# Kernel optimization log

Measured on AMD Instinct MI355X. Metric: run time of the kernel, lower is better.

The kernel has to match this reference:

```python
import jax, jax.numpy as jnp
import numpy as np

D_MODEL = 1024
SEQ_LEN = 32768


def setup_inputs() -> dict:
    key = jax.random.key(0)
    k1, k2, k3 = jax.random.split(key, 3)
    inputs = jax.random.normal(k1, (SEQ_LEN,), dtype=jnp.float32)
    W = jax.random.normal(k2, (D_MODEL, D_MODEL), dtype=jnp.float32) * (1.0 / np.sqrt(D_MODEL))
    b = jax.random.normal(k3, (D_MODEL,), dtype=jnp.float32) * 0.01
    return {"inputs": inputs, "W": W, "b": b}


def reference(inputs, W, b):
    d_model = W.shape[0]
    # t: [D], p: [L] -- log(1 + position)
    t = jnp.linspace(0.0, 1.0, d_model, dtype=inputs.dtype)
    p = jnp.log1p(jnp.arange(inputs.shape[0], dtype=inputs.dtype))
    # phase[l, d] = 2*pi * inputs[l] * (t[d] + p[l]); sum sin over positions
    phase = 2.0 * jnp.pi * inputs[:, None] * (t[None, :] + p[:, None])  # [L, D]
    signal = jnp.sum(jnp.sin(phase), axis=0)  # [D]
    # nn.Linear: x @ W.T + b
    return signal @ W.T + b
```

## Files before the change

### kernel.cpp

```cpp
#include <hip/hip_runtime.h>

#define L_TOTAL 32768
#define D_MODEL 1024
#define LCHUNK  64
#define NQ      (D_MODEL / 256)
#define NBLK_S  ((L_TOTAL / LCHUNK) * NQ)

__global__ __launch_bounds__(256) void signal_kernel(const float* __restrict__ x,
                                                     float* __restrict__ signal) {
    __shared__ float2 sxp[LCHUNK];
    const int tid   = threadIdx.x;
    const int q     = blockIdx.x & (NQ - 1);
    const int c     = blockIdx.x >> 2;
    const int lbase = c * LCHUNK;

    if (tid < LCHUNK) {
        const int l   = lbase + tid;
        const float xv = x[l];
        sxp[tid] = make_float2(xv, xv * __logf(1.0f + (float)l));
    }
    __syncthreads();

    const int   d = q * 256 + tid;
    const float t = (float)d * (1.0f / 1023.0f);

    float a0 = 0.f, a1 = 0.f, a2 = 0.f, a3 = 0.f;
    #pragma unroll
    for (int j = 0; j < LCHUNK; j += 4) {
        const float2 v0 = sxp[j + 0];
        const float2 v1 = sxp[j + 1];
        const float2 v2 = sxp[j + 2];
        const float2 v3 = sxp[j + 3];
        a0 += __builtin_amdgcn_sinf(__builtin_amdgcn_fractf(fmaf(v0.x, t, v0.y)));
        a1 += __builtin_amdgcn_sinf(__builtin_amdgcn_fractf(fmaf(v1.x, t, v1.y)));
        a2 += __builtin_amdgcn_sinf(__builtin_amdgcn_fractf(fmaf(v2.x, t, v2.y)));
        a3 += __builtin_amdgcn_sinf(__builtin_amdgcn_fractf(fmaf(v3.x, t, v3.y)));
    }
    atomicAdd(&signal[d], (a0 + a1) + (a2 + a3));
}

__global__ __launch_bounds__(256) void matvec_kernel(const float* __restrict__ W,
                                                     const float* __restrict__ b,
                                                     const float* __restrict__ signal,
                                                     float* __restrict__ out) {
    const int wave = threadIdx.x >> 6;
    const int lane = threadIdx.x & 63;
    const int row  = blockIdx.x * 4 + wave;

    const float4* Wr = (const float4*)(W + (size_t)row * D_MODEL);
    const float4* S  = (const float4*)signal;

    float sum = 0.f;
    #pragma unroll
    for (int k = 0; k < 4; ++k) {
        const float4 w4 = Wr[lane + 64 * k];
        const float4 s4 = S[lane + 64 * k];
        sum += w4.x * s4.x + w4.y * s4.y + w4.z * s4.z + w4.w * s4.w;
    }
    #pragma unroll
    for (int off = 32; off > 0; off >>= 1)
        sum += __shfl_down(sum, off, 64);
    if (lane == 0) out[row] = sum + b[row];
}

extern "C" void kernel_launch(void* const* d_in, const int* in_sizes, int n_in,
                              void* d_out, int out_size, void* d_ws, size_t ws_size,
                              hipStream_t stream) {
    const float* x = (const float*)d_in[0];
    const float* W = (const float*)d_in[1];
    const float* b = (const float*)d_in[2];
    float* out    = (float*)d_out;
    float* signal = (float*)d_ws;

    hipMemsetAsync(signal, 0, D_MODEL * sizeof(float), stream);
    signal_kernel<<<NBLK_S, 256, 0, stream>>>(x, signal);
    matvec_kernel<<<D_MODEL / 4, 256, 0, stream>>>(W, b, signal, out);
}
```

Measured before the change: 76.57 us.

## Replace atomic accumulation with partial-sum buffer plus deterministic reduce kernel

The signal kernel now writes per-chunk partial sums to a workspace buffer instead of issuing atomicAdds. A new reduce kernel sums those partials per output dimension. This also removes the memset. Chunk size doubles to halve the number of partials, and the matvec splits each row across two waves with 512-thread blocks. The cost is an extra kernel launch plus about 1 MB of partial-sum traffic. The larger chunk also halves the signal-kernel grid, which reduces parallelism.

```diff
diff --git a/kernel.cpp b/kernel.cpp
--- a/kernel.cpp
+++ b/kernel.cpp
@@ -2,12 +2,13 @@
 
 #define L_TOTAL 32768
 #define D_MODEL 1024
-#define LCHUNK  64
+#define LCHUNK  128
+#define NCH     (L_TOTAL / LCHUNK)
 #define NQ      (D_MODEL / 256)
-#define NBLK_S  ((L_TOTAL / LCHUNK) * NQ)
+#define NBLK_S  (NCH * NQ)
 
 __global__ __launch_bounds__(256) void signal_kernel(const float* __restrict__ x,
-                                                     float* __restrict__ signal) {
+                                                     float* __restrict__ part) {
     __shared__ float2 sxp[LCHUNK];
     const int tid   = threadIdx.x;
     const int q     = blockIdx.x & (NQ - 1);
@@ -36,23 +37,43 @@
         a2 += __builtin_amdgcn_sinf(__builtin_amdgcn_fractf(fmaf(v2.x, t, v2.y)));
         a3 += __builtin_amdgcn_sinf(__builtin_amdgcn_fractf(fmaf(v3.x, t, v3.y)));
     }
-    atomicAdd(&signal[d], (a0 + a1) + (a2 + a3));
+    part[c * D_MODEL + d] = (a0 + a1) + (a2 + a3);
 }
 
-__global__ __launch_bounds__(256) void matvec_kernel(const float* __restrict__ W,
+__global__ __launch_bounds__(256) void reduce_kernel(const float* __restrict__ part,
+                                                     float* __restrict__ signal) {
+    __shared__ float red[4][64];
+    const int tid = threadIdx.x;
+    const int dd  = blockIdx.x * 64 + (tid & 63);
+    const int s   = tid >> 6;
+    float acc = 0.f;
+    #pragma unroll 8
+    for (int j = 0; j < NCH / 4; ++j)
+        acc += part[(s * (NCH / 4) + j) * D_MODEL + dd];
+    red[s][tid & 63] = acc;
+    __syncthreads();
+    if (tid < 64)
+        signal[blockIdx.x * 64 + tid] =
+            (red[0][tid] + red[1][tid]) + (red[2][tid] + red[3][tid]);
+}
+
+__global__ __launch_bounds__(512) void matvec_kernel(const float* __restrict__ W,
                                                      const float* __restrict__ b,
                                                      const float* __restrict__ signal,
                                                      float* __restrict__ out) {
-    const int wave = threadIdx.x >> 6;
-    const int lane = threadIdx.x & 63;
-    const int row  = blockIdx.x * 4 + wave;
+    __shared__ float rsum[8];
+    const int tid  = threadIdx.x;
+    const int wv   = tid >> 6;
+    const int lane = tid & 63;
+    const int row  = blockIdx.x * 4 + (wv >> 1);
+    const int h    = wv & 1;
 
     const float4* Wr = (const float4*)(W + (size_t)row * D_MODEL);
     const float4* S  = (const float4*)signal;
 
     float sum = 0.f;
     #pragma unroll
-    for (int k = 0; k < 4; ++k) {
+    for (int k = h * 2; k < h * 2 + 2; ++k) {
         const float4 w4 = Wr[lane + 64 * k];
         const float4 s4 = S[lane + 64 * k];
         sum += w4.x * s4.x + w4.y * s4.y + w4.z * s4.z + w4.w * s4.w;
@@ -60,7 +81,12 @@
     #pragma unroll
     for (int off = 32; off > 0; off >>= 1)
         sum += __shfl_down(sum, off, 64);
-    if (lane == 0) out[row] = sum + b[row];
+    if (lane == 0) rsum[wv] = sum;
+    __syncthreads();
+    if (tid < 4) {
+        const int r = blockIdx.x * 4 + tid;
+        out[r] = rsum[2 * tid] + rsum[2 * tid + 1] + b[r];
+    }
 }
 
 extern "C" void kernel_launch(void* const* d_in, const int* in_sizes, int n_in,
@@ -70,9 +96,10 @@
     const float* W = (const float*)d_in[1];
     const float* b = (const float*)d_in[2];
     float* out    = (float*)d_out;
-    float* signal = (float*)d_ws;
+    float* part   = (float*)d_ws;
+    float* signal = part + NCH * D_MODEL;
 
-    hipMemsetAsync(signal, 0, D_MODEL * sizeof(float), stream);
-    signal_kernel<<<NBLK_S, 256, 0, stream>>>(x, signal);
-    matvec_kernel<<<D_MODEL / 4, 256, 0, stream>>>(W, b, signal, out);
+    signal_kernel<<<NBLK_S, 256, 0, stream>>>(x, part);
+    reduce_kernel<<<D_MODEL / 64, 256, 0, stream>>>(part, signal);
+    matvec_kernel<<<D_MODEL / 4, 512, 0, stream>>>(W, b, signal, out);
 }
```

Measured after the change: 70.41 us. 1.09x faster.

## Fuse signal and matvec into one persistent kernel with grid barriers

Applied to the files above, without the earlier changes.

Replaces the memset, the atomic-accumulating signal kernel and the separate matvec kernel with a single launch of 512 blocks of 512 threads. Blocks write per-chunk partial sums to workspace, and after a software grid barrier half the blocks reduce the partials deterministically into the signal vector. After a second barrier every block computes two output rows, with W rows prefetched before the first barrier. This removes launch overhead and atomics, but relies on all 512 blocks being co-resident and adds a global partial buffer round trip plus spin-wait barriers.

```diff
diff --git a/kernel.cpp b/kernel.cpp
--- a/kernel.cpp
+++ b/kernel.cpp
@@ -2,31 +2,59 @@
 
 #define L_TOTAL 32768
 #define D_MODEL 1024
-#define LCHUNK  64
-#define NQ      (D_MODEL / 256)
-#define NBLK_S  ((L_TOTAL / LCHUNK) * NQ)
+#define NBLK    512
+#define NTHR    512
+#define LCH     128
+#define NCH     (L_TOTAL / LCH)
 
-__global__ __launch_bounds__(256) void signal_kernel(const float* __restrict__ x,
-                                                     float* __restrict__ signal) {
-    __shared__ float2 sxp[LCHUNK];
-    const int tid   = threadIdx.x;
-    const int q     = blockIdx.x & (NQ - 1);
-    const int c     = blockIdx.x >> 2;
-    const int lbase = c * LCHUNK;
+__device__ unsigned int g_bar = 0u;
 
-    if (tid < LCHUNK) {
-        const int l   = lbase + tid;
+__device__ __forceinline__ void grid_sync() {
+    __syncthreads();
+    if (threadIdx.x == 0) {
+        const unsigned int ticket =
+            __hip_atomic_fetch_add(&g_bar, 1u, __ATOMIC_RELEASE, __HIP_MEMORY_SCOPE_AGENT);
+        const unsigned int target = (ticket & ~(unsigned int)(NBLK - 1)) + NBLK;
+        while ((int)(__hip_atomic_load(&g_bar, __ATOMIC_RELAXED,
+                                       __HIP_MEMORY_SCOPE_AGENT) - target) < 0)
+            __builtin_amdgcn_s_sleep(2);
+        __builtin_amdgcn_fence(__ATOMIC_ACQUIRE, "agent");
+    }
+    __syncthreads();
+}
+
+__global__ __launch_bounds__(NTHR, 4) void fused_kernel(const float* __restrict__ x,
+                                                        const float* __restrict__ W,
+                                                        const float* __restrict__ b,
+                                                        float* __restrict__ out,
+                                                        float* __restrict__ ws) {
+    __shared__ float2 sxp[LCH];
+    __shared__ float  wsum[8][4];
+    __shared__ float  rsum[8];
+
+    float* part   = ws;
+    float* signal = ws + NCH * D_MODEL;
+
+    const int tid  = threadIdx.x;
+    const int blk  = blockIdx.x;
+    const int lane = tid & 63;
+    const int wv   = tid >> 6;
+
+    const int c = blk >> 1;
+    const int h = blk & 1;
+    if (tid < LCH) {
+        const int l = c * LCH + tid;
         const float xv = x[l];
         sxp[tid] = make_float2(xv, xv * __logf(1.0f + (float)l));
     }
     __syncthreads();
 
-    const int   d = q * 256 + tid;
+    const int   d = h * 512 + tid;
     const float t = (float)d * (1.0f / 1023.0f);
 
     float a0 = 0.f, a1 = 0.f, a2 = 0.f, a3 = 0.f;
     #pragma unroll
-    for (int j = 0; j < LCHUNK; j += 4) {
+    for (int j = 0; j < LCH; j += 4) {
         const float2 v0 = sxp[j + 0];
         const float2 v1 = sxp[j + 1];
         const float2 v2 = sxp[j + 2];
@@ -36,31 +64,47 @@
         a2 += __builtin_amdgcn_sinf(__builtin_amdgcn_fractf(fmaf(v2.x, t, v2.y)));
         a3 += __builtin_amdgcn_sinf(__builtin_amdgcn_fractf(fmaf(v3.x, t, v3.y)));
     }
-    atomicAdd(&signal[d], (a0 + a1) + (a2 + a3));
-}
+    part[c * D_MODEL + d] = (a0 + a1) + (a2 + a3);
 
-__global__ __launch_bounds__(256) void matvec_kernel(const float* __restrict__ W,
-                                                     const float* __restrict__ b,
-                                                     const float* __restrict__ signal,
-                                                     float* __restrict__ out) {
-    const int wave = threadIdx.x >> 6;
-    const int lane = threadIdx.x & 63;
-    const int row  = blockIdx.x * 4 + wave;
+    const int   q    = wv & 3;
+    const int   row  = 2 * blk + (wv >> 2);
+    const float4 w4  = ((const float4*)(W + (size_t)row * D_MODEL))[q * 64 + lane];
 
-    const float4* Wr = (const float4*)(W + (size_t)row * D_MODEL);
-    const float4* S  = (const float4*)signal;
+    grid_sync();
 
-    float sum = 0.f;
-    #pragma unroll
-    for (int k = 0; k < 4; ++k) {
-        const float4 w4 = Wr[lane + 64 * k];
-        const float4 s4 = S[lane + 64 * k];
-        sum += w4.x * s4.x + w4.y * s4.y + w4.z * s4.z + w4.w * s4.w;
+    if (blk < NBLK / 2) {
+        const int d0 = blk * 4;
+        const int di = tid & 3;
+        const int c0 = tid >> 2;
+        float a = part[c0 * D_MODEL + d0 + di]
+                + part[(c0 + 128) * D_MODEL + d0 + di];
+        a += __shfl_xor(a, 4, 64);
+        a += __shfl_xor(a, 8, 64);
+        a += __shfl_xor(a, 16, 64);
+        a += __shfl_xor(a, 32, 64);
+        if (lane < 4) wsum[wv][lane] = a;
+        __syncthreads();
+        if (tid < 4)
+            signal[d0 + tid] = ((wsum[0][tid] + wsum[1][tid]) +
+                                (wsum[2][tid] + wsum[3][tid])) +
+                               ((wsum[4][tid] + wsum[5][tid]) +
+                                (wsum[6][tid] + wsum[7][tid]));
     }
+
+    grid_sync();
+
+    const float4 s4 = ((const float4*)signal)[q * 64 + lane];
+    float sum = w4.x * s4.x + w4.y * s4.y + w4.z * s4.z + w4.w * s4.w;
     #pragma unroll
     for (int off = 32; off > 0; off >>= 1)
         sum += __shfl_down(sum, off, 64);
-    if (lane == 0) out[row] = sum + b[row];
+    if (lane == 0) rsum[wv] = sum;
+    __syncthreads();
+    if (tid < 2) {
+        const int r = 2 * blk + tid;
+        out[r] = ((rsum[4 * tid] + rsum[4 * tid + 1]) +
+                  (rsum[4 * tid + 2] + rsum[4 * tid + 3])) + b[r];
+    }
 }
 
 extern "C" void kernel_launch(void* const* d_in, const int* in_sizes, int n_in,
@@ -70,9 +114,7 @@
     const float* W = (const float*)d_in[1];
     const float* b = (const float*)d_in[2];
     float* out    = (float*)d_out;
-    float* signal = (float*)d_ws;
+    float* ws     = (float*)d_ws;
 
-    hipMemsetAsync(signal, 0, D_MODEL * sizeof(float), stream);
-    signal_kernel<<<NBLK_S, 256, 0, stream>>>(x, signal);
-    matvec_kernel<<<D_MODEL / 4, 256, 0, stream>>>(W, b, signal, out);
+    fused_kernel<<<NBLK, NTHR, 0, stream>>>(x, W, b, out, ws);
 }
```

Result: slower. 126.5 us (+65.2%).

## Replace atomic signal accumulation with per-chunk partials reduced in matvec kernel

Applied to the files above, without the earlier changes.

The signal kernel now gives each block 512 positions and 128 d-values, and splits the positions across two halves of the block. It writes per-chunk partial sums to workspace instead of issuing global atomicAdds, which removes the memset launch and the atomic contention. The matvec kernel now reduces the 64 partials per d in every block before doing the dot product. This is redundant work across 256 blocks, and it drops the grid from 2048 to 512 blocks.

```diff
diff --git a/kernel.cpp b/kernel.cpp
--- a/kernel.cpp
+++ b/kernel.cpp
@@ -2,65 +2,102 @@
 
 #define L_TOTAL 32768
 #define D_MODEL 1024
-#define LCHUNK  64
-#define NQ      (D_MODEL / 256)
-#define NBLK_S  ((L_TOTAL / LCHUNK) * NQ)
+#define NCH     64
+#define LCH     (L_TOTAL / NCH)
+#define NBLK_S  (NCH * 8)
 
 __global__ __launch_bounds__(256) void signal_kernel(const float* __restrict__ x,
-                                                     float* __restrict__ signal) {
-    __shared__ float2 sxp[LCHUNK];
-    const int tid   = threadIdx.x;
-    const int q     = blockIdx.x & (NQ - 1);
-    const int c     = blockIdx.x >> 2;
-    const int lbase = c * LCHUNK;
+                                                     float* __restrict__ part) {
+    __shared__ float2 sxp[LCH];
+    __shared__ float  hred[256];
+    const int tid = threadIdx.x;
+    const int c   = blockIdx.x >> 3;
+    const int q   = blockIdx.x & 7;
 
-    if (tid < LCHUNK) {
-        const int l   = lbase + tid;
-        const float xv = x[l];
-        sxp[tid] = make_float2(xv, xv * __logf(1.0f + (float)l));
+    {
+        const int l0 = c * LCH + tid;
+        const float x0 = x[l0], x1 = x[l0 + 256];
+        sxp[tid]       = make_float2(x0, x0 * __logf(1.0f + (float)l0));
+        sxp[tid + 256] = make_float2(x1, x1 * __logf(1.0f + (float)(l0 + 256)));
     }
     __syncthreads();
 
-    const int   d = q * 256 + tid;
-    const float t = (float)d * (1.0f / 1023.0f);
+    const int   dl = tid & 127;
+    const int   h  = tid >> 7;
+    const float t  = (float)(q * 128 + dl) * (1.0f / 1023.0f);
 
     float a0 = 0.f, a1 = 0.f, a2 = 0.f, a3 = 0.f;
-    #pragma unroll
-    for (int j = 0; j < LCHUNK; j += 4) {
-        const float2 v0 = sxp[j + 0];
-        const float2 v1 = sxp[j + 1];
-        const float2 v2 = sxp[j + 2];
-        const float2 v3 = sxp[j + 3];
+    #pragma unroll 4
+    for (int j = 0; j < 256; j += 4) {
+        const float2 v0 = sxp[h * 256 + j + 0];
+        const float2 v1 = sxp[h * 256 + j + 1];
+        const float2 v2 = sxp[h * 256 + j + 2];
+        const float2 v3 = sxp[h * 256 + j + 3];
         a0 += __builtin_amdgcn_sinf(__builtin_amdgcn_fractf(fmaf(v0.x, t, v0.y)));
         a1 += __builtin_amdgcn_sinf(__builtin_amdgcn_fractf(fmaf(v1.x, t, v1.y)));
         a2 += __builtin_amdgcn_sinf(__builtin_amdgcn_fractf(fmaf(v2.x, t, v2.y)));
         a3 += __builtin_amdgcn_sinf(__builtin_amdgcn_fractf(fmaf(v3.x, t, v3.y)));
     }
-    atomicAdd(&signal[d], (a0 + a1) + (a2 + a3));
+    hred[tid] = (a0 + a1) + (a2 + a3);
+    __syncthreads();
+    if (tid < 128)
+        part[c * D_MODEL + q * 128 + tid] = hred[tid] + hred[128 + tid];
 }
 
-__global__ __launch_bounds__(256) void matvec_kernel(const float* __restrict__ W,
-                                                     const float* __restrict__ b,
-                                                     const float* __restrict__ signal,
-                                                     float* __restrict__ out) {
-    const int wave = threadIdx.x >> 6;
-    const int lane = threadIdx.x & 63;
-    const int row  = blockIdx.x * 4 + wave;
+__global__ __launch_bounds__(1024) void finish_kernel(const float* __restrict__ W,
+                                                      const float* __restrict__ b,
+                                                      const float* __restrict__ part,
+                                                      float* __restrict__ out) {
+    __shared__ float4 red[4][256];
+    __shared__ float4 ssig[256];
+    __shared__ float  rsum[16];
 
-    const float4* Wr = (const float4*)(W + (size_t)row * D_MODEL);
-    const float4* S  = (const float4*)signal;
+    const int tid = threadIdx.x;
+    const int blk = blockIdx.x;
 
-    float sum = 0.f;
-    #pragma unroll
-    for (int k = 0; k < 4; ++k) {
-        const float4 w4 = Wr[lane + 64 * k];
-        const float4 s4 = S[lane + 64 * k];
-        sum += w4.x * s4.x + w4.y * s4.y + w4.z * s4.z + w4.w * s4.w;
+    {
+        const int dq = tid & 255;
+        const int cs = tid >> 8;
+        const float4* p4 = (const float4*)part;
+        float4 A = make_float4(0.f, 0.f, 0.f, 0.f);
+        float4 B = make_float4(0.f, 0.f, 0.f, 0.f);
+        #pragma unroll
+        for (int j = 0; j < 16; j += 2) {
+            const float4 u = p4[(cs * 16 + j) * 256 + dq];
+            const float4 v = p4[(cs * 16 + j + 1) * 256 + dq];
+            A.x += u.x; A.y += u.y; A.z += u.z; A.w += u.w;
+            B.x += v.x; B.y += v.y; B.z += v.z; B.w += v.w;
+        }
+        A.x += B.x; A.y += B.y; A.z += B.z; A.w += B.w;
+        red[cs][dq] = A;
     }
+    __syncthreads();
+    if (tid < 256) {
+        const float4 r0 = red[0][tid], r1 = red[1][tid];
+        const float4 r2 = red[2][tid], r3 = red[3][tid];
+        ssig[tid] = make_float4((r0.x + r1.x) + (r2.x + r3.x),
+                                (r0.y + r1.y) + (r2.y + r3.y),
+                                (r0.z + r1.z) + (r2.z + r3.z),
+                                (r0.w + r1.w) + (r2.w + r3.w));
+    }
+    __syncthreads();
+
+    const int  wv   = tid >> 6;
+    const int  lane = tid & 63;
+    const int  q    = wv & 3;
+    const int  rl   = wv >> 2;
+    const int  row  = blk * 4 + rl;
+    const float4 w4 = ((const float4*)(W + (size_t)row * D_MODEL))[q * 64 + lane];
+    const float4 s4 = ssig[q * 64 + lane];
+    float sum = w4.x * s4.x + w4.y * s4.y + w4.z * s4.z + w4.w * s4.w;
     #pragma unroll
     for (int off = 32; off > 0; off >>= 1)
         sum += __shfl_down(sum, off, 64);
-    if (lane == 0) out[row] = sum + b[row];
+    if (lane == 0) rsum[wv] = sum;
+    __syncthreads();
+    if (tid < 4)
+        out[blk * 4 + tid] = ((rsum[tid * 4] + rsum[tid * 4 + 1]) +
+                              (rsum[tid * 4 + 2] + rsum[tid * 4 + 3])) + b[blk * 4 + tid];
 }
 
 extern "C" void kernel_launch(void* const* d_in, const int* in_sizes, int n_in,
@@ -70,9 +107,8 @@
     const float* W = (const float*)d_in[1];
     const float* b = (const float*)d_in[2];
     float* out    = (float*)d_out;
-    float* signal = (float*)d_ws;
+    float* part   = (float*)d_ws;
 
-    hipMemsetAsync(signal, 0, D_MODEL * sizeof(float), stream);
-    signal_kernel<<<NBLK_S, 256, 0, stream>>>(x, signal);
-    matvec_kernel<<<D_MODEL / 4, 256, 0, stream>>>(W, b, signal, out);
+    signal_kernel<<<NBLK_S, 256, 0, stream>>>(x, part);
+    finish_kernel<<<D_MODEL / 4, 1024, 0, stream>>>(W, b, part, out);
 }
```

Measured after the change: 68.75 us. -10.2%, faster.
